# Kernel optimization log

Measured on AMD Instinct MI355X. Metric: run time of the kernel, lower is better.

The kernel has to match this reference:

```python
import jax, jax.numpy as jnp
import numpy as np
import math

B, CH, BINS, W = 2, 8, 1024, 1024
FF = 2048
BANDS = 4
HD = BINS // BANDS
EPS = 1e-5


def _ln(x, g, b):
    m = jnp.mean(x, -1, keepdims=True)
    v = jnp.mean(jnp.square(x - m), -1, keepdims=True)
    return (x - m) * jax.lax.rsqrt(v + EPS) * g + b


def _conv1d(x, w, pad, groups=1):
    # x: [B, C, W], w: [O, I/groups, k]
    return jax.lax.conv_general_dilated(x, w, (1,), [(pad, pad)],
                                        dimension_numbers=('NCH', 'OIH', 'NCH'),
                                        feature_group_count=groups)


def _attn(h, mem, qw, qb, qcw, qcb, kw, kb, kcw, kcb, vw, vb, vcw, vcb, ow, ob, er):
    b, w, c = h.shape

    def proj(src, lw, lb, cw, cb):
        y = src @ lw.T + lb                                   # [b, w, c]
        y = _conv1d(y.transpose(0, 2, 1), cw, 1, groups=c) + cb[None, :, None]
        return y.transpose(0, 2, 1)                           # [b, w, c]

    q = proj(h, qw, qb, qcw, qcb).reshape(b, w, BANDS, HD).transpose(0, 2, 1, 3)   # [b, n, w, hd]
    k = proj(mem, kw, kb, kcw, kcb).reshape(b, w, BANDS, HD).transpose(0, 2, 1, 3)
    v = proj(mem, vw, vb, vcw, vcb).reshape(b, w, BANDS, HD).transpose(0, 2, 1, 3)
    # relative position bias via Music-Transformer pad/skew trick
    p = jnp.einsum('bnwh,hc->bnwc', q, er)                    # [b, n, w, W]
    p = jnp.pad(p, ((0, 0), (0, 0), (0, 0), (1, 0))).transpose(0, 1, 3, 2)[:, :, 1:, :]
    qk = (jnp.einsum('bnqh,bnkh->bnqk', q, k) + p) / math.sqrt(c)
    a = jax.nn.softmax(qk, axis=-1)
    o = jnp.einsum('bnqk,bnkh->bnqh', a, v).transpose(0, 2, 1, 3).reshape(b, w, c)
    return o @ ow.T + ob


def _forward(x, w_in, ln1_g, ln1_b, glu_w, ln2_g, ln2_b, c1L_w, c1R_w, ln3_g, ln3_b,
             c1M_dw, c1M_pw, ln4_g, ln4_b, qw, qb, qcw, qcb, kw, kb, kcw, kcb,
             vw, vb, vcw, vcb, ow, ob, er, ln5_g, ln5_b, c2_w, c3_w):
    # in_project: Linear(channels, 1, bias=False) on x.transpose(1,3), squeeze
    xf = jnp.einsum('bcfw,c->bwf', x, w_in)                   # [B, W, BINS]
    # GLU block
    h = _ln(xf, ln1_g, ln1_b)
    g = h @ glu_w.T
    ga, gb = jnp.split(g, 2, axis=-1)
    xf = xf + ga * jax.nn.sigmoid(gb)
    # conv feedforward block
    h = _ln(xf, ln2_g, ln2_b)
    hL = jax.nn.relu(h @ c1L_w.T)                             # [B, W, FF]
    hR = jax.nn.relu(_conv1d(h.transpose(0, 2, 1), c1R_w, 1)).transpose(0, 2, 1)  # [B, W, FF//4]
    hR = jnp.pad(hR, ((0, 0), (0, 0), (0, FF - FF // 4)))
    h = _ln(hL + hR, ln3_g, ln3_b)
    h = _conv1d(_conv1d(h.transpose(0, 2, 1), c1M_dw, 4, groups=FF), c1M_pw, 0).transpose(0, 2, 1)
    xf = xf + h
    # multiband attention
    h = _ln(xf, ln4_g, ln4_b)
    h = _attn(h, h, qw, qb, qcw, qcb, kw, kb, kcw, kcb, vw, vb, vcw, vcb, ow, ob, er)
    xf = xf + h
    # squared-relu FFN
    h = _ln(xf, ln5_g, ln5_b)
    h = jnp.square(jax.nn.relu(h @ c2_w.T)) @ c3_w.T
    xf = xf + h
    return xf.transpose(0, 2, 1)[:, None, :, :]               # [B, 1, BINS, W]


def setup_inputs() -> dict:
    key = jax.random.key(0)
    keys = iter(jax.random.split(key, 48))

    def n(shape, s=0.02):
        return jax.random.normal(next(keys), shape, dtype=jnp.float32) * s

    ones = lambda d: jnp.ones((d,), jnp.float32)
    zeros = lambda d: jnp.zeros((d,), jnp.float32)
    return {
        'x': jax.random.normal(next(keys), (B, CH, BINS, W), dtype=jnp.float32),
        'w_in': n((CH,)),
        'ln1_g': ones(BINS), 'ln1_b': zeros(BINS),
        'glu_w': n((2 * BINS, BINS)),
        'ln2_g': ones(BINS), 'ln2_b': zeros(BINS),
        'c1L_w': n((FF, BINS)),
        'c1R_w': n((FF // 4, BINS, 3)),
        'ln3_g': ones(FF), 'ln3_b': zeros(FF),
        'c1M_dw': n((FF, 1, 9)),
        'c1M_pw': n((BINS, FF, 1)),
        'ln4_g': ones(BINS), 'ln4_b': zeros(BINS),
        'qw': n((BINS, BINS)), 'qb': zeros(BINS), 'qcw': n((BINS, 1, 3)), 'qcb': zeros(BINS),
        'kw': n((BINS, BINS)), 'kb': zeros(BINS), 'kcw': n((BINS, 1, 3)), 'kcb': zeros(BINS),
        'vw': n((BINS, BINS)), 'vb': zeros(BINS), 'vcw': n((BINS, 1, 3)), 'vcb': zeros(BINS),
        'ow': n((BINS, BINS)), 'ob': zeros(BINS),
        'er': n((HD, W), s=1.0),
        'ln5_g': ones(BINS), 'ln5_b': zeros(BINS),
        'c2_w': n((FF, BINS)), 'c3_w': n((BINS, FF)),
    }


def reference(x, w_in, ln1_g, ln1_b, glu_w, ln2_g, ln2_b, c1L_w, c1R_w, ln3_g, ln3_b,
              c1M_dw, c1M_pw, ln4_g, ln4_b, qw, qb, qcw, qcb, kw, kb, kcw, kcb,
              vw, vb, vcw, vcb, ow, ob, er, ln5_g, ln5_b, c2_w, c3_w):
    return _forward(x, w_in, ln1_g, ln1_b, glu_w, ln2_g, ln2_b, c1L_w, c1R_w, ln3_g, ln3_b,
                    c1M_dw, c1M_pw, ln4_g, ln4_b, qw, qb, qcw, qcb, kw, kb, kcw, kcb,
                    vw, vb, vcw, vcb, ow, ob, er, ln5_g, ln5_b, c2_w, c3_w)
```

## Files before the change

kernel.cpp:

```cpp
#include <hip/hip_runtime.h>


typedef float f32x4 __attribute__((ext_vector_type(4)));
typedef short short8 __attribute__((ext_vector_type(8)));
typedef unsigned short u16;
typedef unsigned int u32;

__device__ __forceinline__ float bf2f(u16 u){
  u32 v = ((u32)u) << 16;
  return __builtin_bit_cast(float, v);
}
__device__ __forceinline__ u16 f2bf(float f){
  u32 u = __builtin_bit_cast(u32, f);
  u32 r = (u + 0x7fffu + ((u >> 16) & 1u)) >> 16;
  return (u16)r;
}
__device__ __forceinline__ u32 pack2(float a, float b){
  return (u32)f2bf(a) | ((u32)f2bf(b) << 16);
}
__device__ __forceinline__ void unpack8(uint4 u, float* f){
  f[0]=bf2f(u.x & 0xffffu); f[1]=bf2f(u.x >> 16);
  f[2]=bf2f(u.y & 0xffffu); f[3]=bf2f(u.y >> 16);
  f[4]=bf2f(u.z & 0xffffu); f[5]=bf2f(u.z >> 16);
  f[6]=bf2f(u.w & 0xffffu); f[7]=bf2f(u.w >> 16);
}

__device__ __forceinline__ void gload16(const u16* g, u16* l){
  __builtin_amdgcn_global_load_lds(
      (const __attribute__((address_space(1))) unsigned int*)g,
      (__attribute__((address_space(3))) unsigned int*)l, 16, 0, 0);
}
template<int N> __device__ __forceinline__ void waitvm(){
  asm volatile("s_waitcnt vmcnt(%0)" :: "n"(N) : "memory");
}
__device__ __forceinline__ void barrier(){ __builtin_amdgcn_s_barrier(); }

template<int ACT, int OB, int MR, int NR, int DUAL, int NBUF, int RB, int SC>
__global__ __launch_bounds__(256)
void gemm_bt(const u16* __restrict__ A, const u16* __restrict__ Bw,
             const u16* __restrict__ A2, const u16* __restrict__ B2,
             float* __restrict__ Cf, u16* __restrict__ Cb,
             const float* __restrict__ bias, const void* __restrict__ resid,
             int M, int N, int K, int K2,
             int lda, int ldb, int lda2, int ldb2, int ldc,
             int apad, int aoff,
             long aZHi, long aZLo, long bZHi, long bZLo,
             long b2ZHi, long b2ZLo, long cZHi, long cZLo)
{
  constexpr int BM = 32 * MR, BN = 32 * NR;
  constexpr int LPT = MR + NR;
  constexpr int PRE = NBUF - 1;
  __shared__ __align__(16) u16 As[NBUF][BM * 64];
  __shared__ __align__(16) u16 Bs[NBUF][BN * 64];
  const int z = blockIdx.z, zh = z >> 2, zl = z & 3;
  const u16* Az = A + zh * aZHi + zl * aZLo;
  const u16* Bz = Bw + zh * bZHi + zl * bZLo;
  const u16* B2z = DUAL ? (B2 + zh * b2ZHi + zl * b2ZLo) : nullptr;
  const long coff = (long)zh * cZHi + (long)zl * cZLo;
  const int tid = threadIdx.x;
  const int m0 = blockIdx.y * BM, n0 = blockIdx.x * BN;
  const int lane = tid & 63, wid = tid >> 6;
  const int wm = wid >> 1, wn = wid & 1;
  const int lr = lane & 15, lk = lane >> 4;
  const int kA = K >> 6;
  const int NT = kA + (DUAL ? (K2 >> 6) : 0);

  auto stage = [&](int buf, int s){
    #pragma unroll
    for (int i = 0; i < MR; i++){
      int ch = tid + i * 256;
      if (MR == 1 && ch >= 256) break;
      int r = ch >> 3, c = ch & 7;
      int csw = (c ^ (r & 7)) * 8;
      const u16* src;
      bool d2 = DUAL && (s >= kA);
      if (d2){
        src = A2 + (long)(m0 + r) * lda2 + (s - kA) * 64 + csw;
      } else {
        int gm = m0 + r;
        long ar = (long)gm + (long)(gm >> 10) * apad + aoff;
        src = Az + ar * lda + s * 64 + csw;
      }
      gload16(src, &As[buf][ch * 8]);
    }
    #pragma unroll
    for (int i = 0; i < NR; i++){
      int ch = tid + i * 256;
      int r = ch >> 3, c = ch & 7;
      int csw = (c ^ (r & 7)) * 8;
      const u16* src;
      bool d2 = DUAL && (s >= kA);
      if (d2) src = B2z + (long)(n0 + r) * ldb2 + (s - kA) * 64 + csw;
      else    src = Bz  + (long)(n0 + r) * ldb  + s * 64 + csw;
      gload16(src, &Bs[buf][ch * 8]);
    }
  };

  f32x4 acc[MR][NR];
  #pragma unroll
  for (int i = 0; i < MR; i++)
    #pragma unroll
    for (int j = 0; j < NR; j++) acc[i][j] = f32x4{0.f, 0.f, 0.f, 0.f};

  auto compute = [&](int cur){
    const u16* Ab = &As[cur][0];
    const u16* Bb = &Bs[cur][0];
    short8 av[2][MR], bv[2][NR];
    #pragma unroll
    for (int h = 0; h < 2; h++){
      int g = h * 4 + lk;
      #pragma unroll
      for (int i = 0; i < MR; i++){
        int row = wm * 16 * MR + i * 16 + lr;
        av[h][i] = *(const short8*)(Ab + row * 64 + ((g ^ (row & 7)) * 8));
      }
      #pragma unroll
      for (int j = 0; j < NR; j++){
        int row = wn * 16 * NR + j * 16 + lr;
        bv[h][j] = *(const short8*)(Bb + row * 64 + ((g ^ (row & 7)) * 8));
      }
    }
    #pragma unroll
    for (int h = 0; h < 2; h++)
      #pragma unroll
      for (int i = 0; i < MR; i++)
        #pragma unroll
        for (int j = 0; j < NR; j++)
          acc[i][j] = __builtin_amdgcn_mfma_f32_16x16x32_bf16(av[h][i], bv[h][j], acc[i][j], 0, 0, 0);
  };

  const int npre = NT < PRE ? NT : PRE;
  for (int p = 0; p < npre; p++) stage(p, p);
  int s = 0;
  for (; s < NT - PRE; s++){
    waitvm<(NBUF - 2) * LPT>();
    barrier();
    stage((s + PRE) % NBUF, s + PRE);
    compute(s % NBUF);
  }
  for (; s < NT; s++){
    waitvm<0>();
    barrier();
    compute(s % NBUF);
  }

  float* CfZ = Cf ? Cf + coff : nullptr;
  u16*  CbZ = Cb ? Cb + coff : nullptr;
  const float* rzf = (!RB && resid) ? ((const float*)resid) + coff : nullptr;
  const u16*  rzb = (RB && resid) ? ((const u16*)resid) + coff : nullptr;
  #pragma unroll
  for (int i = 0; i < MR; i++){
    int rowb = m0 + wm * 16 * MR + i * 16 + lk * 4;
    #pragma unroll
    for (int j = 0; j < NR; j++){
      int colg = n0 + wn * 16 * NR + j * 16 + lr;
      f32x4 v = acc[i][j];
      float bvl = bias ? bias[colg] : 0.f;
      #pragma unroll
      for (int r = 0; r < 4; r++){
        long idx = (long)(rowb + r) * ldc + colg;
        float xv = v[r] + bvl;
        if constexpr (ACT == 1){ xv = fmaxf(xv, 0.f); }
        if constexpr (ACT == 2){ xv = fmaxf(xv, 0.f); xv = xv * xv; }
        if constexpr (SC){ xv *= 0.03125f; }
        if constexpr (RB){ if (rzb) xv += bf2f(rzb[idx]); }
        else             { if (rzf) xv += rzf[idx]; }
        if constexpr (OB) CbZ[idx] = f2bf(xv); else CfZ[idx] = xv;
      }
    }
  }
}

template<int NBUF>
__global__ __launch_bounds__(256)
void gemm_glu(const u16* __restrict__ A, const u16* __restrict__ Bw,
              u16* __restrict__ XF)
{
  constexpr int LPT = 6;
  constexpr int PRE = NBUF - 1;
  constexpr int NT = 16;
  __shared__ __align__(16) u16 As[NBUF][64 * 64];
  __shared__ __align__(16) u16 Bs[NBUF][128 * 64];
  const int tid = threadIdx.x;
  const int m0 = blockIdx.y * 64, n0 = blockIdx.x * 64;
  const int lane = tid & 63, wid = tid >> 6;
  const int wm = wid >> 1, wn = wid & 1;
  const int lr = lane & 15, lk = lane >> 4;

  auto stage = [&](int buf, int s){
    #pragma unroll
    for (int i = 0; i < 2; i++){
      int ch = tid + i * 256;
      int r = ch >> 3, c = ch & 7;
      int csw = (c ^ (r & 7)) * 8;
      gload16(A + (long)(m0 + r) * 1024 + s * 64 + csw, &As[buf][ch * 8]);
    }
    #pragma unroll
    for (int i = 0; i < 4; i++){
      int ch = tid + i * 256;
      int r = ch >> 3, c = ch & 7;
      int csw = (c ^ (r & 7)) * 8;
      int grow = (r < 64) ? (n0 + r) : (1024 + n0 + r - 64);
      gload16(Bw + (long)grow * 1024 + s * 64 + csw, &Bs[buf][ch * 8]);
    }
  };

  f32x4 accv[2][2], accg[2][2];
  #pragma unroll
  for (int i = 0; i < 2; i++)
    #pragma unroll
    for (int j = 0; j < 2; j++){
      accv[i][j] = f32x4{0.f,0.f,0.f,0.f};
      accg[i][j] = f32x4{0.f,0.f,0.f,0.f};
    }

  auto compute = [&](int cur){
    const u16* Ab = &As[cur][0];
    const u16* Bb = &Bs[cur][0];
    short8 av[2][2], bvv[2][2], bvg[2][2];
    #pragma unroll
    for (int h = 0; h < 2; h++){
      int g = h * 4 + lk;
      #pragma unroll
      for (int i = 0; i < 2; i++){
        int row = wm * 32 + i * 16 + lr;
        av[h][i] = *(const short8*)(Ab + row * 64 + ((g ^ (row & 7)) * 8));
      }
      #pragma unroll
      for (int j = 0; j < 2; j++){
        int row = wn * 32 + j * 16 + lr;
        bvv[h][j] = *(const short8*)(Bb + row * 64 + ((g ^ (row & 7)) * 8));
        int rowg = 64 + row;
        bvg[h][j] = *(const short8*)(Bb + rowg * 64 + ((g ^ (rowg & 7)) * 8));
      }
    }
    #pragma unroll
    for (int h = 0; h < 2; h++)
      #pragma unroll
      for (int i = 0; i < 2; i++)
        #pragma unroll
        for (int j = 0; j < 2; j++){
          accv[i][j] = __builtin_amdgcn_mfma_f32_16x16x32_bf16(av[h][i], bvv[h][j], accv[i][j], 0, 0, 0);
          accg[i][j] = __builtin_amdgcn_mfma_f32_16x16x32_bf16(av[h][i], bvg[h][j], accg[i][j], 0, 0, 0);
        }
  };

  const int npre = NT < PRE ? NT : PRE;
  for (int p = 0; p < npre; p++) stage(p, p);
  int s = 0;
  for (; s < NT - PRE; s++){
    waitvm<(NBUF - 2) * LPT>();
    barrier();
    stage((s + PRE) % NBUF, s + PRE);
    compute(s % NBUF);
  }
  for (; s < NT; s++){
    waitvm<0>();
    barrier();
    compute(s % NBUF);
  }

  #pragma unroll
  for (int i = 0; i < 2; i++){
    int rowb = m0 + wm * 32 + i * 16 + lk * 4;
    #pragma unroll
    for (int j = 0; j < 2; j++){
      int colg = n0 + wn * 32 + j * 16 + lr;
      #pragma unroll
      for (int r = 0; r < 4; r++){
        long idx = (long)(rowb + r) * 1024 + colg;
        float g = accg[i][j][r];
        float nv = bf2f(XF[idx]) + accv[i][j][r] / (1.f + __expf(-g));
        XF[idx] = f2bf(nv);
      }
    }
  }
}

template<int NC, int INBF>
__global__ __launch_bounds__(256)
void ln_kernel(const void* __restrict__ in, u16* __restrict__ out,
               const float* __restrict__ gg, const float* __restrict__ bb,
               int rowpad, int rowadd)
{
  constexpr int PER = NC / 256;
  const int row = blockIdx.x;
  const int tid = threadIdx.x;
  float v[PER];
  if constexpr (INBF){
    const u16* x = ((const u16*)in) + (long)row * NC + tid * PER;
    if constexpr (PER == 4){
      uint2 u = *(const uint2*)x;
      v[0]=bf2f(u.x & 0xffffu); v[1]=bf2f(u.x >> 16);
      v[2]=bf2f(u.y & 0xffffu); v[3]=bf2f(u.y >> 16);
    } else {
      #pragma unroll
      for (int i = 0; i < PER; i += 8){
        uint4 u = *(const uint4*)(x + i);
        unpack8(u, &v[i]);
      }
    }
  } else {
    const float* x = ((const float*)in) + (long)row * NC + tid * PER;
    #pragma unroll
    for (int i = 0; i < PER; i += 4){
      f32x4 t = *(const f32x4*)(x + i);
      v[i] = t.x; v[i+1] = t.y; v[i+2] = t.z; v[i+3] = t.w;
    }
  }
  float s = 0.f, sq = 0.f;
  #pragma unroll
  for (int i = 0; i < PER; i++){ s += v[i]; sq += v[i] * v[i]; }
  #pragma unroll
  for (int o = 32; o; o >>= 1){ s += __shfl_xor(s, o); sq += __shfl_xor(sq, o); }
  __shared__ float as_[4], aq_[4];
  const int wv = tid >> 6;
  if ((tid & 63) == 0){ as_[wv] = s; aq_[wv] = sq; }
  __syncthreads();
  s  = as_[0] + as_[1] + as_[2] + as_[3];
  sq = aq_[0] + aq_[1] + aq_[2] + aq_[3];
  const float mean = s * (1.f / NC);
  const float var  = sq * (1.f / NC) - mean * mean;
  const float rs = rsqrtf(var + 1e-5f);
  const long orow = (long)row + (long)(row >> 10) * rowpad + rowadd;
  u16* op = out + orow * NC + tid * PER;
  u32 word[PER / 2];
  #pragma unroll
  for (int i = 0; i < PER; i += 2){
    int c = tid * PER + i;
    float y0 = (v[i]   - mean) * rs * gg[c]   + bb[c];
    float y1 = (v[i+1] - mean) * rs * gg[c+1] + bb[c+1];
    word[i / 2] = pack2(y0, y1);
  }
  if constexpr (PER == 4) *(uint2*)op = *(uint2*)word;
  else                    *(uint4*)op = *(uint4*)word;
}

__global__ __launch_bounds__(256)
void inproj_kernel(const float* __restrict__ x, const float* __restrict__ w_in,
                   u16* __restrict__ xf)
{
  __shared__ float tile[32][33];
  const int b = blockIdx.z, f0 = blockIdx.x * 32, w0 = blockIdx.y * 32;
  const int tx = threadIdx.x, ty = threadIdx.y;
  float wr[8];
  #pragma unroll
  for (int c = 0; c < 8; c++) wr[c] = w_in[c];
  #pragma unroll
  for (int i = 0; i < 4; i++){
    int f = f0 + ty + i * 8;
    float s = 0.f;
    #pragma unroll
    for (int c = 0; c < 8; c++)
      s += x[(((long)(b * 8 + c)) * 1024 + f) * 1024 + w0 + tx] * wr[c];
    tile[ty + i * 8][tx] = s;
  }
  __syncthreads();
  #pragma unroll
  for (int i = 0; i < 4; i++){
    int wl = ty + i * 8;
    xf[((long)(b * 1024 + w0 + wl)) * 1024 + f0 + tx] = f2bf(tile[tx][wl]);
  }
}

__global__ __launch_bounds__(256)
void tr_out_kernel(const u16* __restrict__ xf, float* __restrict__ out)
{
  __shared__ float tile[32][33];
  const int b = blockIdx.z, f0 = blockIdx.x * 32, w0 = blockIdx.y * 32;
  const int tx = threadIdx.x, ty = threadIdx.y;
  #pragma unroll
  for (int i = 0; i < 4; i++)
    tile[ty + i * 8][tx] = bf2f(xf[((long)(b * 1024 + w0 + ty + i * 8)) * 1024 + f0 + tx]);
  __syncthreads();
  #pragma unroll
  for (int i = 0; i < 4; i++)
    out[((long)(b * 1024 + f0 + ty + i * 8)) * 1024 + w0 + tx] = tile[tx][ty + i * 8];
}

__global__ __launch_bounds__(256)
void dwconv9_kernel(const u16* __restrict__ in, u16* __restrict__ out,
                    const float* __restrict__ dwT)
{
  const int id = blockIdx.x * 256 + threadIdx.x;
  const int cg = id & 255;
  const int tg = id >> 8;
  const int c0 = cg * 8;
  const int t0 = tg * 4;
  const int b = t0 >> 10;
  const int w0 = t0 & 1023;
  const u16* bin = in + ((long)b << 10) * 2048 + c0;
  float wt[9][8];
  #pragma unroll
  for (int j = 0; j < 9; j++){
    f32x4 lo = *(const f32x4*)(dwT + j * 2048 + c0);
    f32x4 hi = *(const f32x4*)(dwT + j * 2048 + c0 + 4);
    wt[j][0]=lo.x; wt[j][1]=lo.y; wt[j][2]=lo.z; wt[j][3]=lo.w;
    wt[j][4]=hi.x; wt[j][5]=hi.y; wt[j][6]=hi.z; wt[j][7]=hi.w;
  }
  float win[9][8];
  #pragma unroll
  for (int r = 0; r < 9; r++){
    int wr = w0 - 4 + r;
    if (wr >= 0 && wr < 1024){
      uint4 u = *(const uint4*)(bin + (long)wr * 2048);
      unpack8(u, win[r]);
    } else {
      #pragma unroll
      for (int i = 0; i < 8; i++) win[r][i] = 0.f;
    }
  }
  #pragma unroll
  for (int s = 0; s < 4; s++){
    float acc[8] = {0,0,0,0,0,0,0,0};
    #pragma unroll
    for (int j = 0; j < 9; j++)
      #pragma unroll
      for (int i = 0; i < 8; i++)
        acc[i] += win[(s + j) % 9][i] * wt[j][i];
    uint4 o;
    o.x = pack2(acc[0], acc[1]); o.y = pack2(acc[2], acc[3]);
    o.z = pack2(acc[4], acc[5]); o.w = pack2(acc[6], acc[7]);
    *(uint4*)(out + (long)(t0 + s) * 2048 + c0) = o;
    if (s < 3){
      int wr = w0 + s + 5;
      if (wr < 1024){
        uint4 u = *(const uint4*)(bin + (long)wr * 2048);
        unpack8(u, win[s % 9]);
      } else {
        #pragma unroll
        for (int i = 0; i < 8; i++) win[s % 9][i] = 0.f;
      }
    }
  }
}

__global__ __launch_bounds__(256)
void qkvconv_kernel(const u16* __restrict__ qkv,
                    u16* __restrict__ q2b, const float* __restrict__ qwT, const float* __restrict__ qbb,
                    u16* __restrict__ k2b, const float* __restrict__ kwT, const float* __restrict__ kbb,
                    u16* __restrict__ v2T, const float* __restrict__ vcw, const float* __restrict__ vcb)
{
  __shared__ float ins[34][33];
  __shared__ float outs[32][33];
  const int bid = blockIdx.x;
  const int tid = threadIdx.x;
  if (bid < 512){
    const int sel = bid >> 8;
    const u16* in  = qkv + sel * 1024;
    u16* out       = sel ? k2b : q2b;
    const float* wT = sel ? kwT : qwT;
    const float* bp = sel ? kbb : qbb;
    const int id = (bid & 255) * 256 + tid;
    const int cg = id & 127;
    const int tg = id >> 7;
    const int c0 = cg * 8;
    const int t0 = tg * 4;
    const int b = t0 >> 10;
    const int w0 = t0 & 1023;
    const u16* bin = in + ((long)b << 10) * 3072 + c0;
    float wt[3][8], bias[8];
    #pragma unroll
    for (int j = 0; j < 3; j++){
      f32x4 lo = *(const f32x4*)(wT + j * 1024 + c0);
      f32x4 hi = *(const f32x4*)(wT + j * 1024 + c0 + 4);
      wt[j][0]=lo.x; wt[j][1]=lo.y; wt[j][2]=lo.z; wt[j][3]=lo.w;
      wt[j][4]=hi.x; wt[j][5]=hi.y; wt[j][6]=hi.z; wt[j][7]=hi.w;
    }
    {
      f32x4 lo = *(const f32x4*)(bp + c0);
      f32x4 hi = *(const f32x4*)(bp + c0 + 4);
      bias[0]=lo.x; bias[1]=lo.y; bias[2]=lo.z; bias[3]=lo.w;
      bias[4]=hi.x; bias[5]=hi.y; bias[6]=hi.z; bias[7]=hi.w;
    }
    float win[3][8];
    #pragma unroll
    for (int r = 0; r < 3; r++){
      int wr = w0 - 1 + r;
      if (wr >= 0 && wr < 1024){
        uint4 u = *(const uint4*)(bin + (long)wr * 3072);
        unpack8(u, win[r]);
      } else {
        #pragma unroll
        for (int i = 0; i < 8; i++) win[r][i] = 0.f;
      }
    }
    #pragma unroll
    for (int s = 0; s < 4; s++){
      float acc[8];
      #pragma unroll
      for (int i = 0; i < 8; i++) acc[i] = bias[i];
      #pragma unroll
      for (int j = 0; j < 3; j++)
        #pragma unroll
        for (int i = 0; i < 8; i++)
          acc[i] += win[(s + j) % 3][i] * wt[j][i];
      uint4 o;
      o.x = pack2(acc[0], acc[1]); o.y = pack2(acc[2], acc[3]);
      o.z = pack2(acc[4], acc[5]); o.w = pack2(acc[6], acc[7]);
      *(uint4*)(out + (long)(t0 + s) * 1024 + c0) = o;
      if (s < 3){
        int wr = w0 + s + 2;
        if (wr < 1024){
          uint4 u = *(const uint4*)(bin + (long)wr * 3072);
          unpack8(u, win[s % 3]);
        } else {
          #pragma unroll
          for (int i = 0; i < 8; i++) win[s % 3][i] = 0.f;
        }
      }
    }
  } else {
    const int vb = bid - 512;
    const int b = vb >> 10;
    const int rem = vb & 1023;
    const int w0 = (rem & 31) * 32, c0 = (rem >> 5) * 32;
    const int tx = tid & 31, ty = tid >> 5;
    const u16* in = qkv + 2048;
    for (int r = ty; r < 34; r += 8){
      int w = w0 - 1 + r;
      ins[r][tx] = (w >= 0 && w < 1024) ? bf2f(in[((long)(b * 1024 + w)) * 3072 + c0 + tx]) : 0.f;
    }
    __syncthreads();
    const float wt0 = vcw[(c0 + tx) * 3 + 0], wt1 = vcw[(c0 + tx) * 3 + 1], wt2 = vcw[(c0 + tx) * 3 + 2];
    const float bb = vcb[c0 + tx];
    #pragma unroll
    for (int i = 0; i < 4; i++){
      int wl = ty + i * 8;
      outs[wl][tx] = ins[wl][tx] * wt0 + ins[wl + 1][tx] * wt1 + ins[wl + 2][tx] * wt2 + bb;
    }
    __syncthreads();
    #pragma unroll
    for (int i = 0; i < 4; i++){
      int cl = ty + i * 8;
      int c = c0 + cl; int n = c >> 8; int h = c & 255;
      v2T[((long)((b * 4 + n) * 256 + h)) * 1024 + w0 + tx] = f2bf(outs[tx][cl]);
    }
  }
}

__global__ __launch_bounds__(256)
void softmax_kernel(u16* __restrict__ buf)
{
  const long row = (long)blockIdx.x * 4 + (threadIdx.x >> 6);
  const int lane = threadIdx.x & 63;
  u16* p = buf + row * 1024 + lane * 16;
  uint4 a = *(const uint4*)p;
  uint4 b = *(const uint4*)(p + 8);
  float v[16];
  unpack8(a, v); unpack8(b, v + 8);
  float m = v[0];
  #pragma unroll
  for (int i = 1; i < 16; i++) m = fmaxf(m, v[i]);
  #pragma unroll
  for (int o = 32; o; o >>= 1) m = fmaxf(m, __shfl_xor(m, o));
  float e[16];
  float s = 0.f;
  #pragma unroll
  for (int i = 0; i < 16; i++){ e[i] = __expf(v[i] - m); s += e[i]; }
  #pragma unroll
  for (int o = 32; o; o >>= 1) s += __shfl_xor(s, o);
  const float inv = 1.f / s;
  u32 w[8];
  #pragma unroll
  for (int i = 0; i < 16; i += 2) w[i / 2] = pack2(e[i] * inv, e[i + 1] * inv);
  *(uint4*)p = *(uint4*)&w[0];
  *(uint4*)(p + 8) = *(uint4*)&w[4];
}

struct Ptrs9 { const float* s[9]; u16* d[9]; };

__global__ __launch_bounds__(256)
void prep_all_kernel(Ptrs9 p,
                     const float* __restrict__ c1R_w, u16* __restrict__ wb_c1R,
                     const float* __restrict__ er, u16* __restrict__ wb_erT,
                     const float* __restrict__ c1M_dw, float* __restrict__ dwT,
                     const float* __restrict__ qcw, float* __restrict__ qcwT,
                     const float* __restrict__ kcw, float* __restrict__ kcwT,
                     const float* __restrict__ qb, const float* __restrict__ kb,
                     const float* __restrict__ vb, float* __restrict__ bqkv,
                     u16* __restrict__ hpad)
{
  constexpr int n4s[9] = {524288,524288,524288,262144,262144,262144,262144,524288,524288};
  const int tid = threadIdx.x;
  if (blockIdx.x < 18432){
    const int job = blockIdx.x >> 11;
    const int id = (blockIdx.x & 2047) * 256 + tid;
    if (id >= n4s[job]) return;
    f32x4 v = *(const f32x4*)(p.s[job] + (long)id * 4);
    uint2 o; o.x = pack2(v.x, v.y); o.y = pack2(v.z, v.w);
    *(uint2*)(p.d[job] + (long)id * 4) = o;
    return;
  }
  const int bid = blockIdx.x - 18432;
  if (bid < 6144){
    int id = bid * 256 + tid;
    int oc = id / 3072; int rem = id - oc * 3072;
    int tau = rem >> 10; int ic = rem & 1023;
    wb_c1R[id] = f2bf(c1R_w[(long)oc * 3072 + ic * 3 + tau]);
  } else if (bid < 7168){
    int id = (bid - 6144) * 256 + tid;
    int qi = id >> 8; int h = id & 255;
    wb_erT[id] = f2bf(er[(long)h * 1024 + qi]);
  } else if (bid < 7240){
    int id = (bid - 7168) * 256 + tid;
    int jj = id >> 11; int c = id & 2047;
    dwT[id] = c1M_dw[c * 9 + jj];
  } else if (bid < 7252){
    int id = (bid - 7240) * 256 + tid;
    int jj = id >> 10; int c = id & 1023;
    qcwT[id] = qcw[c * 3 + jj];
  } else if (bid < 7264){
    int id = (bid - 7252) * 256 + tid;
    int jj = id >> 10; int c = id & 1023;
    kcwT[id] = kcw[c * 3 + jj];
  } else if (bid < 7276){
    int id = (bid - 7264) * 256 + tid;
    bqkv[id] = (id < 1024) ? qb[id] : (id < 2048) ? kb[id - 1024] : vb[id - 2048];
  } else {
    int id = (bid - 7276) * 256 + tid;
    int r = id >> 10; int c = id & 1023;
    int b = r >> 1; int edge = r & 1;
    long row = (long)b * 1026 + (edge ? 1025 : 0);
    hpad[row * 1024 + c] = 0;
  }
}

extern "C" void kernel_launch(void* const* d_in, const int* in_sizes, int n_in,
                              void* d_out, int out_size, void* d_ws, size_t ws_size,
                              hipStream_t stream)
{
  (void)in_sizes; (void)n_in; (void)out_size; (void)ws_size;
  const float* x     = (const float*)d_in[0];
  const float* w_in  = (const float*)d_in[1];
  const float* ln1_g = (const float*)d_in[2];
  const float* ln1_b = (const float*)d_in[3];
  const float* glu_w = (const float*)d_in[4];
  const float* ln2_g = (const float*)d_in[5];
  const float* ln2_b = (const float*)d_in[6];
  const float* c1L_w = (const float*)d_in[7];
  const float* c1R_w = (const float*)d_in[8];
  const float* ln3_g = (const float*)d_in[9];
  const float* ln3_b = (const float*)d_in[10];
  const float* c1M_dw= (const float*)d_in[11];
  const float* c1M_pw= (const float*)d_in[12];
  const float* ln4_g = (const float*)d_in[13];
  const float* ln4_b = (const float*)d_in[14];
  const float* qw  = (const float*)d_in[15];
  const float* qb  = (const float*)d_in[16];
  const float* qcw = (const float*)d_in[17];
  const float* qcb = (const float*)d_in[18];
  const float* kw  = (const float*)d_in[19];
  const float* kb  = (const float*)d_in[20];
  const float* kcw = (const float*)d_in[21];
  const float* kcb = (const float*)d_in[22];
  const float* vw  = (const float*)d_in[23];
  const float* vb  = (const float*)d_in[24];
  const float* vcw = (const float*)d_in[25];
  const float* vcb = (const float*)d_in[26];
  const float* ow  = (const float*)d_in[27];
  const float* ob  = (const float*)d_in[28];
  const float* er  = (const float*)d_in[29];
  const float* ln5_g = (const float*)d_in[30];
  const float* ln5_b = (const float*)d_in[31];
  const float* c2_w  = (const float*)d_in[32];
  const float* c3_w  = (const float*)d_in[33];
  float* out = (float*)d_out;

  const long TT = 2048;
  char* wsb = (char*)d_ws;
  size_t off = 0;
  auto alloc = [&](size_t bytes) -> char* {
    char* p = wsb + off;
    off = (off + bytes + 255) & ~(size_t)255;
    return p;
  };
  u16* XF     = (u16*)alloc(TT * 1024 * 2);
  u16* wb_glu = (u16*)alloc(2048L * 1024 * 2);
  u16* wb_c1L = (u16*)alloc(2048L * 1024 * 2);
  u16* wb_c1R = (u16*)alloc(512L * 3072 * 2);
  u16* wb_pw  = (u16*)alloc(1024L * 2048 * 2);
  u16* wb_q   = (u16*)alloc(1024L * 1024 * 2);
  u16* wb_k   = (u16*)alloc(1024L * 1024 * 2);
  u16* wb_v   = (u16*)alloc(1024L * 1024 * 2);
  u16* wb_ow  = (u16*)alloc(1024L * 1024 * 2);
  u16* wb_c2  = (u16*)alloc(2048L * 1024 * 2);
  u16* wb_c3  = (u16*)alloc(1024L * 2048 * 2);
  u16* wb_erT = (u16*)alloc(1024L * 256 * 2);
  float* dwT  = (float*)alloc(9L * 2048 * 4);
  float* qcwT = (float*)alloc(3L * 1024 * 4);
  float* kcwT = (float*)alloc(3L * 1024 * 4);
  float* bqkv = (float*)alloc(3072L * 4);
  u16* HPAD   = (u16*)alloc(2L * 1026 * 1024 * 2);
  u16* LNA    = (u16*)alloc(TT * 1024 * 2);
  u16* HS     = (u16*)alloc(TT * 2048 * 2);
  u16* LN3O   = (u16*)alloc(TT * 2048 * 2);
  u16* DW9O   = (u16*)alloc(TT * 2048 * 2);
  u16* SBF    = (u16*)alloc(8L * 1024 * 1024 * 2);
  u16* qkvbuf = (u16*)alloc(TT * 3072 * 2);
  u16* q2b  = (u16*)alloc(TT * 1024 * 2);
  u16* k2b  = (u16*)alloc(TT * 1024 * 2);
  u16* v2T  = (u16*)alloc(8L * 256 * 1024 * 2);
  u16* obuf = qkvbuf;
  u16* C2O  = LN3O;

  Ptrs9 pj;
  pj.s[0]=glu_w; pj.d[0]=wb_glu;
  pj.s[1]=c1L_w; pj.d[1]=wb_c1L;
  pj.s[2]=c1M_pw; pj.d[2]=wb_pw;
  pj.s[3]=qw; pj.d[3]=wb_q;
  pj.s[4]=kw; pj.d[4]=wb_k;
  pj.s[5]=vw; pj.d[5]=wb_v;
  pj.s[6]=ow; pj.d[6]=wb_ow;
  pj.s[7]=c2_w; pj.d[7]=wb_c2;
  pj.s[8]=c3_w; pj.d[8]=wb_c3;
  prep_all_kernel<<<25724, 256, 0, stream>>>(pj, c1R_w, wb_c1R, er, wb_erT, c1M_dw, dwT,
                                             qcw, qcwT, kcw, kcwT, qb, kb, vb, bqkv, HPAD);

  inproj_kernel<<<dim3(32, 32, 2), dim3(32, 8), 0, stream>>>(x, w_in, XF);

  ln_kernel<1024,1><<<2048, 256, 0, stream>>>(XF, LNA, ln1_g, ln1_b, 0, 0);
  gemm_glu<2><<<dim3(16,32,1), 256, 0, stream>>>(LNA, wb_glu, XF);

  ln_kernel<1024,1><<<2048, 256, 0, stream>>>(XF, HPAD, ln2_g, ln2_b, 2, 1);
  gemm_bt<1,1,4,2,0,2,0,0><<<dim3(32,16,1), 256, 0, stream>>>(HPAD, wb_c1L, nullptr, nullptr,
      nullptr, HS, nullptr, nullptr,
      2048, 2048, 1024, 0, 1024, 1024, 0, 0, 2048, 2, 1, 0,0,0,0,0,0,0,0);
  gemm_bt<1,1,2,1,0,4,1,0><<<dim3(16,32,1), 256, 0, stream>>>(HPAD, wb_c1R, nullptr, nullptr,
      nullptr, HS, nullptr, HS,
      2048, 512, 3072, 0, 1024, 3072, 0, 0, 2048, 2, 0, 0,0,0,0,0,0,0,0);
  ln_kernel<2048,1><<<2048, 256, 0, stream>>>(HS, LN3O, ln3_g, ln3_b, 0, 0);
  dwconv9_kernel<<<512, 256, 0, stream>>>(LN3O, DW9O, dwT);
  gemm_bt<0,1,2,2,0,3,1,0><<<dim3(16,32,1), 256, 0, stream>>>(DW9O, wb_pw, nullptr, nullptr,
      nullptr, XF, nullptr, XF,
      2048, 1024, 2048, 0, 2048, 2048, 0, 0, 1024, 0, 0, 0,0,0,0,0,0,0,0);

  ln_kernel<1024,1><<<2048, 256, 0, stream>>>(XF, LNA, ln4_g, ln4_b, 0, 0);
  gemm_bt<0,1,4,2,0,2,0,0><<<dim3(48,16,1), 256, 0, stream>>>(LNA, wb_q, nullptr, nullptr,
      nullptr, qkvbuf, bqkv, nullptr,
      2048, 3072, 1024, 0, 1024, 1024, 0, 0, 3072, 0, 0, 0,0,0,0,0,0,0,0);
  qkvconv_kernel<<<2560, 256, 0, stream>>>(qkvbuf, q2b, qcwT, qcb, k2b, kcwT, kcb,
                                           v2T, vcw, vcb);
  gemm_bt<0,1,2,2,1,3,0,1><<<dim3(16,16,8), 256, 0, stream>>>(q2b, k2b, wb_erT, q2b,
      nullptr, SBF, nullptr, nullptr,
      1024, 1024, 256, 256, 1024, 1024, 256, 1024, 1024, 0, 0,
      1048576, 256, 1048576, 256, 1048576, 256, 4194304, 1048576);
  softmax_kernel<<<2048, 256, 0, stream>>>(SBF);
  gemm_bt<0,1,1,2,0,4,0,0><<<dim3(4,32,8), 256, 0, stream>>>(SBF, v2T, nullptr, nullptr,
      nullptr, obuf, nullptr, nullptr,
      1024, 256, 1024, 0, 1024, 1024, 0, 0, 1024, 0, 0,
      4194304, 1048576, 1048576, 262144, 0, 0, 1048576, 256);
  gemm_bt<0,1,2,2,0,3,1,0><<<dim3(16,32,1), 256, 0, stream>>>(obuf, wb_ow, nullptr, nullptr,
      nullptr, XF, ob, XF,
      2048, 1024, 1024, 0, 1024, 1024, 0, 0, 1024, 0, 0, 0,0,0,0,0,0,0,0);

  ln_kernel<1024,1><<<2048, 256, 0, stream>>>(XF, LNA, ln5_g, ln5_b, 0, 0);
  gemm_bt<2,1,4,2,0,2,0,0><<<dim3(32,16,1), 256, 0, stream>>>(LNA, wb_c2, nullptr, nullptr,
      nullptr, C2O, nullptr, nullptr,
      2048, 2048, 1024, 0, 1024, 1024, 0, 0, 2048, 0, 0, 0,0,0,0,0,0,0,0);
  gemm_bt<0,1,2,2,0,3,1,0><<<dim3(16,32,1), 256, 0, stream>>>(C2O, wb_c3, nullptr, nullptr,
      nullptr, XF, nullptr, XF,
      2048, 1024, 2048, 0, 2048, 2048, 0, 0, 1024, 0, 0, 0,0,0,0,0,0,0,0);

  tr_out_kernel<<<dim3(32, 32, 2), dim3(32, 8), 0, stream>>>(XF, out);
}
```

Measured before the change: 299.3 us.

## Merge c1L/c1R GEMMs into one launch and fold the in-projection into the prep kernel

Moves the GEMM body into a shared device function so a single gemm_c1 kernel can run both the c1L (relu, 1024-wide K) and c1R (3-tap conv as K=3072) tiles under one grid. The c1R output now goes to a separate HR buffer, and LN3 adds it while loading instead of having the c1R GEMM read-modify-write HS. The in-projection transpose kernel is appended as extra blocks of prep_all_kernel. Together these cut two launches and let the small c1R GEMM fill the gaps left by c1L, at the cost of a shared LDS footprint sized for the larger variant, which may reduce occupancy for the c1R tiles.

```diff
diff --git a/kernel.cpp b/kernel.cpp
--- a/kernel.cpp
+++ b/kernel.cpp
@@ -34,6 +34,129 @@
   asm volatile("s_waitcnt vmcnt(%0)" :: "n"(N) : "memory");
 }
 __device__ __forceinline__ void barrier(){ __builtin_amdgcn_s_barrier(); }
+
+template<int ACT, int OB, int MR, int NR, int DUAL, int NBUF, int RB, int SC>
+__device__ __forceinline__
+void gemm_body(u16* ldsA, u16* ldsB,
+               const u16* Az, const u16* Bz,
+               const u16* A2, const u16* B2z,
+               float* CfZ, u16* CbZ,
+               const float* bias, const void* rz,
+               int K, int K2, int lda, int ldb, int lda2, int ldb2, int ldc,
+               int apad, int aoff, int m0, int n0)
+{
+  constexpr int BM = 32 * MR, BN = 32 * NR;
+  constexpr int LPT = MR + NR;
+  constexpr int PRE = NBUF - 1;
+  const int tid = threadIdx.x;
+  const int lane = tid & 63, wid = tid >> 6;
+  const int wm = wid >> 1, wn = wid & 1;
+  const int lr = lane & 15, lk = lane >> 4;
+  const int kA = K >> 6;
+  const int NT = kA + (DUAL ? (K2 >> 6) : 0);
+
+  auto stage = [&](int buf, int s){
+    #pragma unroll
+    for (int i = 0; i < MR; i++){
+      int ch = tid + i * 256;
+      int r = ch >> 3, c = ch & 7;
+      int csw = (c ^ (r & 7)) * 8;
+      const u16* src;
+      bool d2 = DUAL && (s >= kA);
+      if (d2){
+        src = A2 + (long)(m0 + r) * lda2 + (s - kA) * 64 + csw;
+      } else {
+        int gm = m0 + r;
+        long ar = (long)gm + (long)(gm >> 10) * apad + aoff;
+        src = Az + ar * lda + s * 64 + csw;
+      }
+      gload16(src, ldsA + buf * (BM * 64) + ch * 8);
+    }
+    #pragma unroll
+    for (int i = 0; i < NR; i++){
+      int ch = tid + i * 256;
+      int r = ch >> 3, c = ch & 7;
+      int csw = (c ^ (r & 7)) * 8;
+      const u16* src;
+      bool d2 = DUAL && (s >= kA);
+      if (d2) src = B2z + (long)(n0 + r) * ldb2 + (s - kA) * 64 + csw;
+      else    src = Bz  + (long)(n0 + r) * ldb  + s * 64 + csw;
+      gload16(src, ldsB + buf * (BN * 64) + ch * 8);
+    }
+  };
+
+  f32x4 acc[MR][NR];
+  #pragma unroll
+  for (int i = 0; i < MR; i++)
+    #pragma unroll
+    for (int j = 0; j < NR; j++) acc[i][j] = f32x4{0.f, 0.f, 0.f, 0.f};
+
+  auto compute = [&](int cur){
+    const u16* Ab = ldsA + cur * (BM * 64);
+    const u16* Bb = ldsB + cur * (BN * 64);
+    short8 av[2][MR], bv[2][NR];
+    #pragma unroll
+    for (int h = 0; h < 2; h++){
+      int g = h * 4 + lk;
+      #pragma unroll
+      for (int i = 0; i < MR; i++){
+        int row = wm * 16 * MR + i * 16 + lr;
+        av[h][i] = *(const short8*)(Ab + row * 64 + ((g ^ (row & 7)) * 8));
+      }
+      #pragma unroll
+      for (int j = 0; j < NR; j++){
+        int row = wn * 16 * NR + j * 16 + lr;
+        bv[h][j] = *(const short8*)(Bb + row * 64 + ((g ^ (row & 7)) * 8));
+      }
+    }
+    #pragma unroll
+    for (int h = 0; h < 2; h++)
+      #pragma unroll
+      for (int i = 0; i < MR; i++)
+        #pragma unroll
+        for (int j = 0; j < NR; j++)
+          acc[i][j] = __builtin_amdgcn_mfma_f32_16x16x32_bf16(av[h][i], bv[h][j], acc[i][j], 0, 0, 0);
+  };
+
+  const int npre = NT < PRE ? NT : PRE;
+  for (int p = 0; p < npre; p++) stage(p, p);
+  int s = 0;
+  for (; s < NT - PRE; s++){
+    waitvm<(NBUF - 2) * LPT>();
+    barrier();
+    stage((s + PRE) % NBUF, s + PRE);
+    compute(s % NBUF);
+  }
+  for (; s < NT; s++){
+    waitvm<0>();
+    barrier();
+    compute(s % NBUF);
+  }
+
+  const float* rzf = (!RB) ? (const float*)rz : nullptr;
+  const u16*  rzb = ( RB) ? (const u16*)rz  : nullptr;
+  #pragma unroll
+  for (int i = 0; i < MR; i++){
+    int rowb = m0 + wm * 16 * MR + i * 16 + lk * 4;
+    #pragma unroll
+    for (int j = 0; j < NR; j++){
+      int colg = n0 + wn * 16 * NR + j * 16 + lr;
+      f32x4 v = acc[i][j];
+      float bvl = bias ? bias[colg] : 0.f;
+      #pragma unroll
+      for (int r = 0; r < 4; r++){
+        long idx = (long)(rowb + r) * ldc + colg;
+        float xv = v[r] + bvl;
+        if constexpr (ACT == 1){ xv = fmaxf(xv, 0.f); }
+        if constexpr (ACT == 2){ xv = fmaxf(xv, 0.f); xv = xv * xv; }
+        if constexpr (SC){ xv *= 0.03125f; }
+        if constexpr (RB){ if (rzb) xv += bf2f(rzb[idx]); }
+        else             { if (rzf) xv += rzf[idx]; }
+        if constexpr (OB) CbZ[idx] = f2bf(xv); else CfZ[idx] = xv;
+      }
+    }
+  }
+}
 
 template<int ACT, int OB, int MR, int NR, int DUAL, int NBUF, int RB, int SC>
 __global__ __launch_bounds__(256)
@@ -48,126 +171,40 @@
              long b2ZHi, long b2ZLo, long cZHi, long cZLo)
 {
   constexpr int BM = 32 * MR, BN = 32 * NR;
-  constexpr int LPT = MR + NR;
-  constexpr int PRE = NBUF - 1;
-  __shared__ __align__(16) u16 As[NBUF][BM * 64];
-  __shared__ __align__(16) u16 Bs[NBUF][BN * 64];
+  __shared__ __align__(16) u16 As[NBUF * BM * 64];
+  __shared__ __align__(16) u16 Bs[NBUF * BN * 64];
   const int z = blockIdx.z, zh = z >> 2, zl = z & 3;
   const u16* Az = A + zh * aZHi + zl * aZLo;
   const u16* Bz = Bw + zh * bZHi + zl * bZLo;
   const u16* B2z = DUAL ? (B2 + zh * b2ZHi + zl * b2ZLo) : nullptr;
   const long coff = (long)zh * cZHi + (long)zl * cZLo;
-  const int tid = threadIdx.x;
   const int m0 = blockIdx.y * BM, n0 = blockIdx.x * BN;
-  const int lane = tid & 63, wid = tid >> 6;
-  const int wm = wid >> 1, wn = wid & 1;
-  const int lr = lane & 15, lk = lane >> 4;
-  const int kA = K >> 6;
-  const int NT = kA + (DUAL ? (K2 >> 6) : 0);
-
-  auto stage = [&](int buf, int s){
-    #pragma unroll
-    for (int i = 0; i < MR; i++){
-      int ch = tid + i * 256;
-      if (MR == 1 && ch >= 256) break;
-      int r = ch >> 3, c = ch & 7;
-      int csw = (c ^ (r & 7)) * 8;
-      const u16* src;
-      bool d2 = DUAL && (s >= kA);
-      if (d2){
-        src = A2 + (long)(m0 + r) * lda2 + (s - kA) * 64 + csw;
-      } else {
-        int gm = m0 + r;
-        long ar = (long)gm + (long)(gm >> 10) * apad + aoff;
-        src = Az + ar * lda + s * 64 + csw;
-      }
-      gload16(src, &As[buf][ch * 8]);
-    }
-    #pragma unroll
-    for (int i = 0; i < NR; i++){
-      int ch = tid + i * 256;
-      int r = ch >> 3, c = ch & 7;
-      int csw = (c ^ (r & 7)) * 8;
-      const u16* src;
-      bool d2 = DUAL && (s >= kA);
-      if (d2) src = B2z + (long)(n0 + r) * ldb2 + (s - kA) * 64 + csw;
-      else    src = Bz  + (long)(n0 + r) * ldb  + s * 64 + csw;
-      gload16(src, &Bs[buf][ch * 8]);
-    }
-  };
-
-  f32x4 acc[MR][NR];
-  #pragma unroll
-  for (int i = 0; i < MR; i++)
-    #pragma unroll
-    for (int j = 0; j < NR; j++) acc[i][j] = f32x4{0.f, 0.f, 0.f, 0.f};
-
-  auto compute = [&](int cur){
-    const u16* Ab = &As[cur][0];
-    const u16* Bb = &Bs[cur][0];
-    short8 av[2][MR], bv[2][NR];
-    #pragma unroll
-    for (int h = 0; h < 2; h++){
-      int g = h * 4 + lk;
-      #pragma unroll
-      for (int i = 0; i < MR; i++){
-        int row = wm * 16 * MR + i * 16 + lr;
-        av[h][i] = *(const short8*)(Ab + row * 64 + ((g ^ (row & 7)) * 8));
-      }
-      #pragma unroll
-      for (int j = 0; j < NR; j++){
-        int row = wn * 16 * NR + j * 16 + lr;
-        bv[h][j] = *(const short8*)(Bb + row * 64 + ((g ^ (row & 7)) * 8));
-      }
-    }
-    #pragma unroll
-    for (int h = 0; h < 2; h++)
-      #pragma unroll
-      for (int i = 0; i < MR; i++)
-        #pragma unroll
-        for (int j = 0; j < NR; j++)
-          acc[i][j] = __builtin_amdgcn_mfma_f32_16x16x32_bf16(av[h][i], bv[h][j], acc[i][j], 0, 0, 0);
-  };
-
-  const int npre = NT < PRE ? NT : PRE;
-  for (int p = 0; p < npre; p++) stage(p, p);
-  int s = 0;
-  for (; s < NT - PRE; s++){
-    waitvm<(NBUF - 2) * LPT>();
-    barrier();
-    stage((s + PRE) % NBUF, s + PRE);
-    compute(s % NBUF);
-  }
-  for (; s < NT; s++){
-    waitvm<0>();
-    barrier();
-    compute(s % NBUF);
-  }
-
   float* CfZ = Cf ? Cf + coff : nullptr;
   u16*  CbZ = Cb ? Cb + coff : nullptr;
-  const float* rzf = (!RB && resid) ? ((const float*)resid) + coff : nullptr;
-  const u16*  rzb = (RB && resid) ? ((const u16*)resid) + coff : nullptr;
-  #pragma unroll
-  for (int i = 0; i < MR; i++){
-    int rowb = m0 + wm * 16 * MR + i * 16 + lk * 4;
-    #pragma unroll
-    for (int j = 0; j < NR; j++){
-      int colg = n0 + wn * 16 * NR + j * 16 + lr;
-      f32x4 v = acc[i][j];
-      float bvl = bias ? bias[colg] : 0.f;
-      #pragma unroll
-      for (int r = 0; r < 4; r++){
-        long idx = (long)(rowb + r) * ldc + colg;
-        float xv = v[r] + bvl;
-        if constexpr (ACT == 1){ xv = fmaxf(xv, 0.f); }
-        if constexpr (ACT == 2){ xv = fmaxf(xv, 0.f); xv = xv * xv; }
-        if constexpr (SC){ xv *= 0.03125f; }
-        if constexpr (RB){ if (rzb) xv += bf2f(rzb[idx]); }
-        else             { if (rzf) xv += rzf[idx]; }
-        if constexpr (OB) CbZ[idx] = f2bf(xv); else CfZ[idx] = xv;
-      }
-    }
+  const void* rz = nullptr;
+  if (resid) rz = RB ? (const void*)(((const u16*)resid) + coff)
+                     : (const void*)(((const float*)resid) + coff);
+  gemm_body<ACT,OB,MR,NR,DUAL,NBUF,RB,SC>(As, Bs, Az, Bz, A2, B2z, CfZ, CbZ,
+      bias, rz, K, K2, lda, ldb, lda2, ldb2, ldc, apad, aoff, m0, n0);
+}
+
+__global__ __launch_bounds__(256)
+void gemm_c1(const u16* __restrict__ HPAD, const u16* __restrict__ wbL,
+             const u16* __restrict__ wbR, u16* __restrict__ HS, u16* __restrict__ HR)
+{
+  __shared__ __align__(16) u16 lds[24576];
+  const int bid = blockIdx.x;
+  if (bid < 512){
+    const int n0 = (bid & 31) * 64, m0 = (bid >> 5) * 128;
+    gemm_body<1,1,4,2,0,2,0,0>(lds, lds + 2 * 128 * 64,
+        HPAD, wbL, nullptr, nullptr, nullptr, HS, nullptr, nullptr,
+        1024, 0, 1024, 1024, 0, 0, 2048, 2, 1, m0, n0);
+  } else {
+    const int r = bid - 512;
+    const int n0 = (r & 15) * 32, m0 = (r >> 4) * 64;
+    gemm_body<1,1,2,1,0,4,0,0>(lds, lds + 4 * 64 * 64,
+        HPAD, wbR, nullptr, nullptr, nullptr, HR, nullptr, nullptr,
+        3072, 0, 1024, 3072, 0, 0, 512, 2, 0, m0, n0);
   }
 }
 
@@ -277,11 +314,11 @@
   }
 }
 
-template<int NC, int INBF>
+template<int NC, int INBF, int ADDHR>
 __global__ __launch_bounds__(256)
 void ln_kernel(const void* __restrict__ in, u16* __restrict__ out,
                const float* __restrict__ gg, const float* __restrict__ bb,
-               int rowpad, int rowadd)
+               int rowpad, int rowadd, const u16* __restrict__ addp)
 {
   constexpr int PER = NC / 256;
   const int row = blockIdx.x;
@@ -306,6 +343,15 @@
     for (int i = 0; i < PER; i += 4){
       f32x4 t = *(const f32x4*)(x + i);
       v[i] = t.x; v[i+1] = t.y; v[i+2] = t.z; v[i+3] = t.w;
+    }
+  }
+  if constexpr (ADDHR){
+    const int c0i = tid * PER;
+    if (c0i < 512){
+      uint4 u = *(const uint4*)(addp + (long)row * 512 + c0i);
+      float a8[8]; unpack8(u, a8);
+      #pragma unroll
+      for (int i = 0; i < 8; i++) v[i] += a8[i];
     }
   }
   float s = 0.f, sq = 0.f;
@@ -334,33 +380,6 @@
   }
   if constexpr (PER == 4) *(uint2*)op = *(uint2*)word;
   else                    *(uint4*)op = *(uint4*)word;
-}
-
-__global__ __launch_bounds__(256)
-void inproj_kernel(const float* __restrict__ x, const float* __restrict__ w_in,
-                   u16* __restrict__ xf)
-{
-  __shared__ float tile[32][33];
-  const int b = blockIdx.z, f0 = blockIdx.x * 32, w0 = blockIdx.y * 32;
-  const int tx = threadIdx.x, ty = threadIdx.y;
-  float wr[8];
-  #pragma unroll
-  for (int c = 0; c < 8; c++) wr[c] = w_in[c];
-  #pragma unroll
-  for (int i = 0; i < 4; i++){
-    int f = f0 + ty + i * 8;
-    float s = 0.f;
-    #pragma unroll
-    for (int c = 0; c < 8; c++)
-      s += x[(((long)(b * 8 + c)) * 1024 + f) * 1024 + w0 + tx] * wr[c];
-    tile[ty + i * 8][tx] = s;
-  }
-  __syncthreads();
-  #pragma unroll
-  for (int i = 0; i < 4; i++){
-    int wl = ty + i * 8;
-    xf[((long)(b * 1024 + w0 + wl)) * 1024 + f0 + tx] = f2bf(tile[tx][wl]);
-  }
 }
 
 __global__ __launch_bounds__(256)
@@ -579,8 +598,11 @@
                      const float* __restrict__ kcw, float* __restrict__ kcwT,
                      const float* __restrict__ qb, const float* __restrict__ kb,
                      const float* __restrict__ vb, float* __restrict__ bqkv,
-                     u16* __restrict__ hpad)
-{
+                     u16* __restrict__ hpad,
+                     const float* __restrict__ x, const float* __restrict__ w_in,
+                     u16* __restrict__ XF)
+{
+  __shared__ float tile[32][33];
   constexpr int n4s[9] = {524288,524288,524288,262144,262144,262144,262144,524288,524288};
   const int tid = threadIdx.x;
   if (blockIdx.x < 18432){
@@ -617,12 +639,36 @@
   } else if (bid < 7276){
     int id = (bid - 7264) * 256 + tid;
     bqkv[id] = (id < 1024) ? qb[id] : (id < 2048) ? kb[id - 1024] : vb[id - 2048];
-  } else {
+  } else if (bid < 7292){
     int id = (bid - 7276) * 256 + tid;
     int r = id >> 10; int c = id & 1023;
     int b = r >> 1; int edge = r & 1;
     long row = (long)b * 1026 + (edge ? 1025 : 0);
     hpad[row * 1024 + c] = 0;
+  } else {
+    const int vb = bid - 7292;
+    const int b = vb >> 10;
+    const int rem = vb & 1023;
+    const int f0 = (rem & 31) * 32, w0 = (rem >> 5) * 32;
+    const int tx = tid & 31, ty = tid >> 5;
+    float wr[8];
+    #pragma unroll
+    for (int c = 0; c < 8; c++) wr[c] = w_in[c];
+    #pragma unroll
+    for (int i = 0; i < 4; i++){
+      int f = f0 + ty + i * 8;
+      float s = 0.f;
+      #pragma unroll
+      for (int c = 0; c < 8; c++)
+        s += x[(((long)(b * 8 + c)) * 1024 + f) * 1024 + w0 + tx] * wr[c];
+      tile[ty + i * 8][tx] = s;
+    }
+    __syncthreads();
+    #pragma unroll
+    for (int i = 0; i < 4; i++){
+      int wl = ty + i * 8;
+      XF[((long)(b * 1024 + w0 + wl)) * 1024 + f0 + tx] = f2bf(tile[tx][wl]);
+    }
   }
 }
 
@@ -694,6 +740,7 @@
   u16* HPAD   = (u16*)alloc(2L * 1026 * 1024 * 2);
   u16* LNA    = (u16*)alloc(TT * 1024 * 2);
   u16* HS     = (u16*)alloc(TT * 2048 * 2);
+  u16* HR     = (u16*)alloc(TT * 512 * 2);
   u16* LN3O   = (u16*)alloc(TT * 2048 * 2);
   u16* DW9O   = (u16*)alloc(TT * 2048 * 2);
   u16* SBF    = (u16*)alloc(8L * 1024 * 1024 * 2);
@@ -714,28 +761,22 @@
   pj.s[6]=ow; pj.d[6]=wb_ow;
   pj.s[7]=c2_w; pj.d[7]=wb_c2;
   pj.s[8]=c3_w; pj.d[8]=wb_c3;
-  prep_all_kernel<<<25724, 256, 0, stream>>>(pj, c1R_w, wb_c1R, er, wb_erT, c1M_dw, dwT,
-                                             qcw, qcwT, kcw, kcwT, qb, kb, vb, bqkv, HPAD);
-
-  inproj_kernel<<<dim3(32, 32, 2), dim3(32, 8), 0, stream>>>(x, w_in, XF);
-
-  ln_kernel<1024,1><<<2048, 256, 0, stream>>>(XF, LNA, ln1_g, ln1_b, 0, 0);
+  prep_all_kernel<<<27772, 256, 0, stream>>>(pj, c1R_w, wb_c1R, er, wb_erT, c1M_dw, dwT,
+                                             qcw, qcwT, kcw, kcwT, qb, kb, vb, bqkv, HPAD,
+                                             x, w_in, XF);
+
+  ln_kernel<1024,1,0><<<2048, 256, 0, stream>>>(XF, LNA, ln1_g, ln1_b, 0, 0, nullptr);
   gemm_glu<2><<<dim3(16,32,1), 256, 0, stream>>>(LNA, wb_glu, XF);
 
-  ln_kernel<1024,1><<<2048, 256, 0, stream>>>(XF, HPAD, ln2_g, ln2_b, 2, 1);
-  gemm_bt<1,1,4,2,0,2,0,0><<<dim3(32,16,1), 256, 0, stream>>>(HPAD, wb_c1L, nullptr, nullptr,
-      nullptr, HS, nullptr, nullptr,
-      2048, 2048, 1024, 0, 1024, 1024, 0, 0, 2048, 2, 1, 0,0,0,0,0,0,0,0);
-  gemm_bt<1,1,2,1,0,4,1,0><<<dim3(16,32,1), 256, 0, stream>>>(HPAD, wb_c1R, nullptr, nullptr,
-      nullptr, HS, nullptr, HS,
-      2048, 512, 3072, 0, 1024, 3072, 0, 0, 2048, 2, 0, 0,0,0,0,0,0,0,0);
-  ln_kernel<2048,1><<<2048, 256, 0, stream>>>(HS, LN3O, ln3_g, ln3_b, 0, 0);
+  ln_kernel<1024,1,0><<<2048, 256, 0, stream>>>(XF, HPAD, ln2_g, ln2_b, 2, 1, nullptr);
+  gemm_c1<<<1024, 256, 0, stream>>>(HPAD, wb_c1L, wb_c1R, HS, HR);
+  ln_kernel<2048,1,1><<<2048, 256, 0, stream>>>(HS, LN3O, ln3_g, ln3_b, 0, 0, HR);
   dwconv9_kernel<<<512, 256, 0, stream>>>(LN3O, DW9O, dwT);
   gemm_bt<0,1,2,2,0,3,1,0><<<dim3(16,32,1), 256, 0, stream>>>(DW9O, wb_pw, nullptr, nullptr,
       nullptr, XF, nullptr, XF,
       2048, 1024, 2048, 0, 2048, 2048, 0, 0, 1024, 0, 0, 0,0,0,0,0,0,0,0);
 
-  ln_kernel<1024,1><<<2048, 256, 0, stream>>>(XF, LNA, ln4_g, ln4_b, 0, 0);
+  ln_kernel<1024,1,0><<<2048, 256, 0, stream>>>(XF, LNA, ln4_g, ln4_b, 0, 0, nullptr);
   gemm_bt<0,1,4,2,0,2,0,0><<<dim3(48,16,1), 256, 0, stream>>>(LNA, wb_q, nullptr, nullptr,
       nullptr, qkvbuf, bqkv, nullptr,
       2048, 3072, 1024, 0, 1024, 1024, 0, 0, 3072, 0, 0, 0,0,0,0,0,0,0,0);
@@ -754,7 +795,7 @@
       nullptr, XF, ob, XF,
       2048, 1024, 1024, 0, 1024, 1024, 0, 0, 1024, 0, 0, 0,0,0,0,0,0,0,0);
 
-  ln_kernel<1024,1><<<2048, 256, 0, stream>>>(XF, LNA, ln5_g, ln5_b, 0, 0);
+  ln_kernel<1024,1,0><<<2048, 256, 0, stream>>>(XF, LNA, ln5_g, ln5_b, 0, 0, nullptr);
   gemm_bt<2,1,4,2,0,2,0,0><<<dim3(32,16,1), 256, 0, stream>>>(LNA, wb_c2, nullptr, nullptr,
       nullptr, C2O, nullptr, nullptr,
       2048, 2048, 1024, 0, 1024, 1024, 0, 0, 2048, 0, 0, 0,0,0,0,0,0,0,0);
```

Measured after the change: 282.3 us. 5.7% less time.
